# Performance work log

Measured on AMD Instinct MI355X. Metric: run time of the kernel, lower is better.

The kernel has to match this reference:

```python
import jax, jax.numpy as jnp
import numpy as np

BN_EPS = 1e-5

def setup_inputs() -> dict:
    key = jax.random.key(0)
    ks = jax.random.split(key, 8)
    B, C, H, W = 32, 256, 64, 64
    Cm, Co = 128, 256  # mid = max(8, 256//2), out = 256
    x = jax.random.normal(ks[0], (B, C, H, W), dtype=jnp.float32)
    w1 = jax.random.normal(ks[1], (Cm, C), dtype=jnp.float32) * 0.05
    b1 = jnp.zeros((Cm,), dtype=jnp.float32)
    bn_gamma = jnp.ones((Cm,), dtype=jnp.float32)
    bn_beta = jnp.zeros((Cm,), dtype=jnp.float32)
    bn_mean = jnp.zeros((Cm,), dtype=jnp.float32)
    bn_var = jnp.ones((Cm,), dtype=jnp.float32)
    w2 = jax.random.normal(ks[2], (Co, Cm), dtype=jnp.float32) * 0.05
    b2 = jnp.zeros((Co,), dtype=jnp.float32)
    w3 = jax.random.normal(ks[3], (Co, Cm), dtype=jnp.float32) * 0.05
    b3 = jnp.zeros((Co,), dtype=jnp.float32)
    return {"x": x, "w1": w1, "b1": b1, "bn_gamma": bn_gamma, "bn_beta": bn_beta,
            "bn_mean": bn_mean, "bn_var": bn_var, "w2": w2, "b2": b2, "w3": w3, "b3": b3}

def _hswish(y):
    return y * jnp.clip(y + 3.0, 0.0, 6.0) / 6.0

def reference(x, w1, b1, bn_gamma, bn_beta, bn_mean, bn_var, w2, b2, w3, b3):
    B, C, H, W = x.shape
    # pool_h: mean over W -> [B,C,H]; pool_w: mean over H -> [B,C,W] (after permute)
    xh = jnp.mean(x, axis=3)  # [B,C,H]
    xw = jnp.mean(x, axis=2)  # [B,C,W]
    y = jnp.concatenate([xh, xw], axis=2)  # [B,C,H+W]
    # 1x1 conv as matmul over channel dim
    y = jnp.einsum('mc,bcl->bml', w1, y) + b1[None, :, None]  # [B,Cm,H+W]
    # BatchNorm (inference, running stats)
    y = (y - bn_mean[None, :, None]) * (bn_gamma[None, :, None] * jax.lax.rsqrt(bn_var + BN_EPS)[None, :, None]) + bn_beta[None, :, None]
    y = _hswish(y)
    ah, aw = y[:, :, :H], y[:, :, H:]  # [B,Cm,H], [B,Cm,W]
    gh = jax.nn.sigmoid(jnp.einsum('om,bmh->boh', w2, ah) + b2[None, :, None])  # [B,Co,H]
    gw = jax.nn.sigmoid(jnp.einsum('om,bmw->bow', w3, aw) + b3[None, :, None])  # [B,Co,W]
    return x * gh[:, :, :, None] * gw[:, :, None, :]
```

## Files before the change

### kernel.cpp

```cpp
#include <hip/hip_runtime.h>

#define NB 32
#define NC 256
#define NH 64
#define NW 64
#define NCM 128
#define NCO 256
#define NL 128

typedef float v4f __attribute__((ext_vector_type(4)));

__global__ __launch_bounds__(256) void k_pool(const float* __restrict__ x,
                                              float* __restrict__ pool) {
    int plane = blockIdx.x;
    const float4* px = (const float4*)(x + (size_t)plane * 4096);
    int t = threadIdx.x;
    __shared__ float smem[256 * 4];

    float4 csum = make_float4(0.f, 0.f, 0.f, 0.f);
    for (int i = 0; i < 4; ++i) {
        int f = t + i * 256;
        float4 v = px[f];
        csum.x += v.x; csum.y += v.y; csum.z += v.z; csum.w += v.w;
        float s = v.x + v.y + v.z + v.w;
        s += __shfl_xor(s, 1);
        s += __shfl_xor(s, 2);
        s += __shfl_xor(s, 4);
        s += __shfl_xor(s, 8);
        if ((t & 15) == 0) {
            int row = (t >> 4) + 16 * i;
            pool[(size_t)plane * NL + row] = s * 0.015625f;
        }
    }
    ((float4*)smem)[t] = csum;
    __syncthreads();
    if (t < 64) {
        int m = t >> 2, k = t & 3;
        float acc = 0.f;
        #pragma unroll
        for (int g = 0; g < 16; ++g)
            acc += smem[(m + 16 * g) * 4 + k];
        pool[(size_t)plane * NL + 64 + t] = acc * 0.015625f;
    }
}

__global__ __launch_bounds__(256) void k_mlp1(const float* __restrict__ pool,
                                              const float* __restrict__ w1,
                                              const float* __restrict__ b1,
                                              const float* __restrict__ gam,
                                              const float* __restrict__ bet,
                                              const float* __restrict__ mu,
                                              const float* __restrict__ var,
                                              float* __restrict__ a) {
    int b = blockIdx.x, m0 = blockIdx.y * 16;
    int t = threadIdx.x;
    __shared__ float w1t[32][16];
    __shared__ float pt[32][NL];
    const float* poolb = pool + (size_t)b * NC * NL;
    int tm = t & 7;
    int tl = t >> 3;
    float acc[2][4] = {};

    for (int cc = 0; cc < NC; cc += 32) {
        {
            int mi = t & 15, c0 = (t >> 4) * 2;
            float2 wv = *(const float2*)(w1 + (size_t)(m0 + mi) * NC + cc + c0);
            w1t[c0 + 0][mi] = wv.x; w1t[c0 + 1][mi] = wv.y;
        }
        #pragma unroll
        for (int i = 0; i < 4; ++i) {
            int f = t + i * 256;
            int ci = f >> 5, l4 = f & 31;
            *(float4*)&pt[ci][l4 * 4] =
                *(const float4*)(poolb + (size_t)(cc + ci) * NL + l4 * 4);
        }
        __syncthreads();
        #pragma unroll
        for (int cj = 0; cj < 32; ++cj) {
            float2 wv = *(const float2*)&w1t[cj][tm * 2];
            float4 pv = *(const float4*)&pt[cj][tl * 4];
            float wa[2] = {wv.x, wv.y};
            float pa[4] = {pv.x, pv.y, pv.z, pv.w};
            #pragma unroll
            for (int i = 0; i < 2; ++i)
                #pragma unroll
                for (int j = 0; j < 4; ++j)
                    acc[i][j] += wa[i] * pa[j];
        }
        __syncthreads();
    }
    #pragma unroll
    for (int i = 0; i < 2; ++i) {
        int m = m0 + tm * 2 + i;
        float scale = gam[m] * rsqrtf(var[m] + 1e-5f);
        float base = b1[m] - mu[m];
        float bb = bet[m];
        #pragma unroll
        for (int j = 0; j < 4; ++j) {
            float y = (acc[i][j] + base) * scale + bb;
            float hs = y * fminf(fmaxf(y + 3.f, 0.f), 6.f) * (1.f / 6.f);
            a[(size_t)b * NCM * NL + (size_t)m * NL + tl * 4 + j] = hs;
        }
    }
}

__global__ __launch_bounds__(256) void k_gate(const float* __restrict__ a,
                                              const float* __restrict__ w2,
                                              const float* __restrict__ b2,
                                              const float* __restrict__ w3,
                                              const float* __restrict__ b3,
                                              float* __restrict__ gh,
                                              float* __restrict__ gw) {
    int b = blockIdx.x, side = blockIdx.y, ot = blockIdx.z;
    const float* wsel = side ? w3 : w2;
    const float* bsel = side ? b3 : b2;
    float* gsel = side ? gw : gh;
    int t = threadIdx.x;
    __shared__ float wt[32][32];
    __shared__ float at[32][64];
    int to = t & 15;
    int th = t >> 4;
    float acc[2][4] = {};
    const float* ab = a + (size_t)b * NCM * NL + side * 64;

    for (int kc = 0; kc < NCM; kc += 32) {
        {
            int oi = t & 31, k0 = (t >> 5) * 4;
            float4 wv = *(const float4*)(wsel + (size_t)(ot * 32 + oi) * NCM + kc + k0);
            wt[k0 + 0][oi] = wv.x; wt[k0 + 1][oi] = wv.y;
            wt[k0 + 2][oi] = wv.z; wt[k0 + 3][oi] = wv.w;
        }
        #pragma unroll
        for (int i = 0; i < 2; ++i) {
            int f = t + i * 256;
            int ki = f >> 4, h4 = f & 15;
            *(float4*)&at[ki][h4 * 4] =
                *(const float4*)(ab + (size_t)(kc + ki) * NL + h4 * 4);
        }
        __syncthreads();
        #pragma unroll
        for (int kj = 0; kj < 32; ++kj) {
            float2 wv = *(const float2*)&wt[kj][to * 2];
            float4 av = *(const float4*)&at[kj][th * 4];
            float wa[2] = {wv.x, wv.y};
            float aa[4] = {av.x, av.y, av.z, av.w};
            #pragma unroll
            for (int i = 0; i < 2; ++i)
                #pragma unroll
                for (int j = 0; j < 4; ++j)
                    acc[i][j] += wa[i] * aa[j];
        }
        __syncthreads();
    }
    #pragma unroll
    for (int i = 0; i < 2; ++i) {
        int o = ot * 32 + to * 2 + i;
        float bias = bsel[o];
        #pragma unroll
        for (int j = 0; j < 4; ++j) {
            float v = acc[i][j] + bias;
            float g = 1.f / (1.f + __expf(-v));
            gsel[((size_t)b * NCO + o) * 64 + th * 4 + j] = g;
        }
    }
}

__global__ __launch_bounds__(256) void k_apply(const float* __restrict__ x,
                                               const float* __restrict__ gh,
                                               const float* __restrict__ gw,
                                               float* __restrict__ out) {
    int plane = blockIdx.x;
    int t = threadIdx.x;
    const float4* px = (const float4*)(x + (size_t)plane * 4096);
    v4f* po = (v4f*)(out + (size_t)plane * 4096);
    const float* ghp = gh + (size_t)plane * 64;
    const float4* gwp = (const float4*)(gw + (size_t)plane * 64);
    #pragma unroll
    for (int i = 0; i < 4; ++i) {
        int f = t + i * 256;
        int row = f >> 4, w4 = f & 15;
        float4 v = px[f];
        float g = ghp[row];
        float4 gv = gwp[w4];
        v4f r;
        r.x = v.x * g * gv.x; r.y = v.y * g * gv.y;
        r.z = v.z * g * gv.z; r.w = v.w * g * gv.w;
        __builtin_nontemporal_store(r, po + f);
    }
}

extern "C" void kernel_launch(void* const* d_in, const int* in_sizes, int n_in,
                              void* d_out, int out_size, void* d_ws, size_t ws_size,
                              hipStream_t stream) {
    const float* x   = (const float*)d_in[0];
    const float* w1  = (const float*)d_in[1];
    const float* b1  = (const float*)d_in[2];
    const float* gam = (const float*)d_in[3];
    const float* bet = (const float*)d_in[4];
    const float* mu  = (const float*)d_in[5];
    const float* var = (const float*)d_in[6];
    const float* w2  = (const float*)d_in[7];
    const float* b2  = (const float*)d_in[8];
    const float* w3  = (const float*)d_in[9];
    const float* b3  = (const float*)d_in[10];
    float* ws   = (float*)d_ws;
    float* pool = ws;
    float* a    = ws + 1048576;
    float* gh   = ws + 1572864;
    float* gw   = ws + 2097152;
    float* out  = (float*)d_out;

    k_pool<<<NB * NC, 256, 0, stream>>>(x, pool);
    k_mlp1<<<dim3(NB, 8), 256, 0, stream>>>(pool, w1, b1, gam, bet, mu, var, a);
    k_gate<<<dim3(NB, 2, 8), 256, 0, stream>>>(a, w2, b2, w3, b3, gh, gw);
    k_apply<<<NB * NC, 256, 0, stream>>>(x, gh, gw, out);
}
```

Measured before the change: 85.19 us.

## Fuse four stages into one persistent cooperative kernel with grid syncs

Replaces the four separate launches (pool, first MLP, gate, apply) with a single cooperative persistent kernel that loops over work units and separates the stages with grid.sync(). It is meant to remove launch gaps and tail effects between small kernels. The grid is sized from the occupancy query and capped at 1024 blocks, so the small MLP stages run on few blocks and the grid barriers add their own cost. The old multi-kernel path is kept as a fallback if the cooperative launch fails.

```diff
diff --git a/kernel.cpp b/kernel.cpp
--- a/kernel.cpp
+++ b/kernel.cpp
@@ -1,14 +1,187 @@
 #include <hip/hip_runtime.h>
+#include <hip/hip_cooperative_groups.h>
+
+namespace cg = cooperative_groups;
 
 #define NB 32
 #define NC 256
-#define NH 64
-#define NW 64
+#define NL 128
 #define NCM 128
 #define NCO 256
-#define NL 128
+#define NPLANES (NB * NC)
 
 typedef float v4f __attribute__((ext_vector_type(4)));
+
+__global__ __launch_bounds__(256, 4) void k_fused(
+    const float* __restrict__ x,
+    const float* __restrict__ w1, const float* __restrict__ b1,
+    const float* __restrict__ gam, const float* __restrict__ bet,
+    const float* __restrict__ mu, const float* __restrict__ var,
+    const float* __restrict__ w2, const float* __restrict__ b2,
+    const float* __restrict__ w3, const float* __restrict__ b3,
+    float* __restrict__ pool, float* __restrict__ a,
+    float* __restrict__ gh, float* __restrict__ gw,
+    float* __restrict__ out)
+{
+    cg::grid_group grid = cg::this_grid();
+    __shared__ float smem[4608];
+    const int G = gridDim.x;
+    const int blk = blockIdx.x;
+    const int t = threadIdx.x;
+
+    for (int plane = blk; plane < NPLANES; plane += G) {
+        const float4* px = (const float4*)(x + (size_t)plane * 4096);
+        float4 csum = make_float4(0.f, 0.f, 0.f, 0.f);
+        #pragma unroll
+        for (int i = 0; i < 4; ++i) {
+            int f = t + i * 256;
+            float4 v = px[f];
+            csum.x += v.x; csum.y += v.y; csum.z += v.z; csum.w += v.w;
+            float s = v.x + v.y + v.z + v.w;
+            s += __shfl_xor(s, 1);
+            s += __shfl_xor(s, 2);
+            s += __shfl_xor(s, 4);
+            s += __shfl_xor(s, 8);
+            if ((t & 15) == 0)
+                pool[(size_t)plane * NL + (t >> 4) + 16 * i] = s * 0.015625f;
+        }
+        ((float4*)smem)[t] = csum;
+        __syncthreads();
+        if (t < 64) {
+            float acc = 0.f;
+            #pragma unroll
+            for (int g = 0; g < 16; ++g)
+                acc += smem[((t >> 2) + 16 * g) * 4 + (t & 3)];
+            pool[(size_t)plane * NL + 64 + t] = acc * 0.015625f;
+        }
+        __syncthreads();
+    }
+    grid.sync();
+
+    for (int u = blk; u < 256; u += G) {
+        int b = u >> 3, m0 = (u & 7) * 16;
+        float* w1t = smem;
+        float* pt  = smem + 512;
+        const float* poolb = pool + (size_t)b * NC * NL;
+        int tm = t & 7;
+        int tl = t >> 3;
+        float acc[2][4] = {};
+        for (int cc = 0; cc < NC; cc += 32) {
+            {
+                int mi = t & 15, c0 = (t >> 4) * 2;
+                float2 wv = *(const float2*)(w1 + (size_t)(m0 + mi) * NC + cc + c0);
+                w1t[(c0 + 0) * 16 + mi] = wv.x;
+                w1t[(c0 + 1) * 16 + mi] = wv.y;
+            }
+            #pragma unroll
+            for (int i = 0; i < 4; ++i) {
+                int f = t + i * 256;
+                int ci = f >> 5, l4 = f & 31;
+                *(float4*)&pt[ci * 128 + l4 * 4] =
+                    *(const float4*)(poolb + (size_t)(cc + ci) * NL + l4 * 4);
+            }
+            __syncthreads();
+            #pragma unroll
+            for (int cj = 0; cj < 32; ++cj) {
+                float2 wv = *(const float2*)&w1t[cj * 16 + tm * 2];
+                float4 pv = *(const float4*)&pt[cj * 128 + tl * 4];
+                float pa[4] = {pv.x, pv.y, pv.z, pv.w};
+                #pragma unroll
+                for (int j = 0; j < 4; ++j) {
+                    acc[0][j] += wv.x * pa[j];
+                    acc[1][j] += wv.y * pa[j];
+                }
+            }
+            __syncthreads();
+        }
+        #pragma unroll
+        for (int i = 0; i < 2; ++i) {
+            int m = m0 + tm * 2 + i;
+            float scale = gam[m] * rsqrtf(var[m] + 1e-5f);
+            float base = b1[m] - mu[m];
+            float bb = bet[m];
+            #pragma unroll
+            for (int j = 0; j < 4; ++j) {
+                float y = (acc[i][j] + base) * scale + bb;
+                float hs = y * fminf(fmaxf(y + 3.f, 0.f), 6.f) * (1.f / 6.f);
+                a[(size_t)b * NCM * NL + (size_t)m * NL + tl * 4 + j] = hs;
+            }
+        }
+    }
+    grid.sync();
+
+    for (int u = blk; u < 512; u += G) {
+        int b = u >> 4, side = (u >> 3) & 1, ot = u & 7;
+        const float* wsel = side ? w3 : w2;
+        const float* bsel = side ? b3 : b2;
+        float* gsel = side ? gw : gh;
+        float* wt = smem;
+        float* at = smem + 1024;
+        int to = t & 15;
+        int th = t >> 4;
+        float acc[2][4] = {};
+        const float* ab = a + (size_t)b * NCM * NL + side * 64;
+        for (int kc = 0; kc < NCM; kc += 32) {
+            {
+                int oi = t & 31, k0 = (t >> 5) * 4;
+                float4 wv = *(const float4*)(wsel + (size_t)(ot * 32 + oi) * NCM + kc + k0);
+                wt[(k0 + 0) * 32 + oi] = wv.x; wt[(k0 + 1) * 32 + oi] = wv.y;
+                wt[(k0 + 2) * 32 + oi] = wv.z; wt[(k0 + 3) * 32 + oi] = wv.w;
+            }
+            #pragma unroll
+            for (int i = 0; i < 2; ++i) {
+                int f = t + i * 256;
+                int ki = f >> 4, h4 = f & 15;
+                *(float4*)&at[ki * 64 + h4 * 4] =
+                    *(const float4*)(ab + (size_t)(kc + ki) * NL + h4 * 4);
+            }
+            __syncthreads();
+            #pragma unroll
+            for (int kj = 0; kj < 32; ++kj) {
+                float2 wv = *(const float2*)&wt[kj * 32 + to * 2];
+                float4 av = *(const float4*)&at[kj * 64 + th * 4];
+                float aa[4] = {av.x, av.y, av.z, av.w};
+                #pragma unroll
+                for (int j = 0; j < 4; ++j) {
+                    acc[0][j] += wv.x * aa[j];
+                    acc[1][j] += wv.y * aa[j];
+                }
+            }
+            __syncthreads();
+        }
+        #pragma unroll
+        for (int i = 0; i < 2; ++i) {
+            int o = ot * 32 + to * 2 + i;
+            float bias = bsel[o];
+            #pragma unroll
+            for (int j = 0; j < 4; ++j) {
+                float v = acc[i][j] + bias;
+                float g = 1.f / (1.f + __expf(-v));
+                gsel[((size_t)b * NCO + o) * 64 + th * 4 + j] = g;
+            }
+        }
+    }
+    grid.sync();
+
+    for (int plane = blk; plane < NPLANES; plane += G) {
+        const float4* px = (const float4*)(x + (size_t)plane * 4096);
+        v4f* po = (v4f*)(out + (size_t)plane * 4096);
+        const float* ghp = gh + (size_t)plane * 64;
+        const float4* gwp = (const float4*)(gw + (size_t)plane * 64);
+        #pragma unroll
+        for (int i = 0; i < 4; ++i) {
+            int f = t + i * 256;
+            int row = f >> 4, w4 = f & 15;
+            float4 v = px[f];
+            float g = ghp[row];
+            float4 gv = gwp[w4];
+            v4f r;
+            r.x = v.x * g * gv.x; r.y = v.y * g * gv.y;
+            r.z = v.z * g * gv.z; r.w = v.w * g * gv.w;
+            __builtin_nontemporal_store(r, po + f);
+        }
+    }
+}
 
 __global__ __launch_bounds__(256) void k_pool(const float* __restrict__ x,
                                               float* __restrict__ pool) {
@@ -16,7 +189,6 @@
     const float4* px = (const float4*)(x + (size_t)plane * 4096);
     int t = threadIdx.x;
     __shared__ float smem[256 * 4];
-
     float4 csum = make_float4(0.f, 0.f, 0.f, 0.f);
     for (int i = 0; i < 4; ++i) {
         int f = t + i * 256;
@@ -27,19 +199,16 @@
         s += __shfl_xor(s, 2);
         s += __shfl_xor(s, 4);
         s += __shfl_xor(s, 8);
-        if ((t & 15) == 0) {
-            int row = (t >> 4) + 16 * i;
-            pool[(size_t)plane * NL + row] = s * 0.015625f;
-        }
+        if ((t & 15) == 0)
+            pool[(size_t)plane * NL + (t >> 4) + 16 * i] = s * 0.015625f;
     }
     ((float4*)smem)[t] = csum;
     __syncthreads();
     if (t < 64) {
-        int m = t >> 2, k = t & 3;
         float acc = 0.f;
         #pragma unroll
         for (int g = 0; g < 16; ++g)
-            acc += smem[(m + 16 * g) * 4 + k];
+            acc += smem[((t >> 2) + 16 * g) * 4 + (t & 3)];
         pool[(size_t)plane * NL + 64 + t] = acc * 0.015625f;
     }
 }
@@ -57,10 +226,8 @@
     __shared__ float w1t[32][16];
     __shared__ float pt[32][NL];
     const float* poolb = pool + (size_t)b * NC * NL;
-    int tm = t & 7;
-    int tl = t >> 3;
+    int tm = t & 7, tl = t >> 3;
     float acc[2][4] = {};
-
     for (int cc = 0; cc < NC; cc += 32) {
         {
             int mi = t & 15, c0 = (t >> 4) * 2;
@@ -79,13 +246,12 @@
         for (int cj = 0; cj < 32; ++cj) {
             float2 wv = *(const float2*)&w1t[cj][tm * 2];
             float4 pv = *(const float4*)&pt[cj][tl * 4];
-            float wa[2] = {wv.x, wv.y};
             float pa[4] = {pv.x, pv.y, pv.z, pv.w};
             #pragma unroll
-            for (int i = 0; i < 2; ++i)
-                #pragma unroll
-                for (int j = 0; j < 4; ++j)
-                    acc[i][j] += wa[i] * pa[j];
+            for (int j = 0; j < 4; ++j) {
+                acc[0][j] += wv.x * pa[j];
+                acc[1][j] += wv.y * pa[j];
+            }
         }
         __syncthreads();
     }
@@ -118,11 +284,9 @@
     int t = threadIdx.x;
     __shared__ float wt[32][32];
     __shared__ float at[32][64];
-    int to = t & 15;
-    int th = t >> 4;
+    int to = t & 15, th = t >> 4;
     float acc[2][4] = {};
     const float* ab = a + (size_t)b * NCM * NL + side * 64;
-
     for (int kc = 0; kc < NCM; kc += 32) {
         {
             int oi = t & 31, k0 = (t >> 5) * 4;
@@ -142,13 +306,12 @@
         for (int kj = 0; kj < 32; ++kj) {
             float2 wv = *(const float2*)&wt[kj][to * 2];
             float4 av = *(const float4*)&at[kj][th * 4];
-            float wa[2] = {wv.x, wv.y};
             float aa[4] = {av.x, av.y, av.z, av.w};
             #pragma unroll
-            for (int i = 0; i < 2; ++i)
-                #pragma unroll
-                for (int j = 0; j < 4; ++j)
-                    acc[i][j] += wa[i] * aa[j];
+            for (int j = 0; j < 4; ++j) {
+                acc[0][j] += wv.x * aa[j];
+                acc[1][j] += wv.y * aa[j];
+            }
         }
         __syncthreads();
     }
@@ -210,8 +373,22 @@
     float* gw   = ws + 2097152;
     float* out  = (float*)d_out;
 
-    k_pool<<<NB * NC, 256, 0, stream>>>(x, pool);
-    k_mlp1<<<dim3(NB, 8), 256, 0, stream>>>(pool, w1, b1, gam, bet, mu, var, a);
-    k_gate<<<dim3(NB, 2, 8), 256, 0, stream>>>(a, w2, b2, w3, b3, gh, gw);
-    k_apply<<<NB * NC, 256, 0, stream>>>(x, gh, gw, out);
-}
+    int maxBlk = 0;
+    hipError_t oe = hipOccupancyMaxActiveBlocksPerMultiprocessor(
+        &maxBlk, k_fused, 256, 0);
+    int G = (oe == hipSuccess && maxBlk > 0) ? maxBlk * 256 : 512;
+    if (G > 1024) G = 1024;
+
+    void* args[] = {(void*)&x, (void*)&w1, (void*)&b1, (void*)&gam, (void*)&bet,
+                    (void*)&mu, (void*)&var, (void*)&w2, (void*)&b2, (void*)&w3,
+                    (void*)&b3, (void*)&pool, (void*)&a, (void*)&gh, (void*)&gw,
+                    (void*)&out};
+    hipError_t le = hipLaunchCooperativeKernel((const void*)k_fused, dim3(G),
+                                               dim3(256), args, 0, stream);
+    if (le != hipSuccess) {
+        k_pool<<<NPLANES, 256, 0, stream>>>(x, pool);
+        k_mlp1<<<dim3(NB, 8), 256, 0, stream>>>(pool, w1, b1, gam, bet, mu, var, a);
+        k_gate<<<dim3(NB, 2, 8), 256, 0, stream>>>(a, w2, b2, w3, b3, gh, gw);
+        k_apply<<<NPLANES, 256, 0, stream>>>(x, gh, gw, out);
+    }
+}
```

After: 246.9 us. 190% more time.
